# Kernel optimization log

Hardware: AMD Instinct MI355X
Metric: run time of the kernel (lower is better)

## Reference

```python
import jax, jax.numpy as jnp
import numpy as np

H, C = 4, 64          # heads, per-head out_channels (hidden_dim // heads)
D = 256               # hidden_dim
DE = 128              # edge_dim
N_ROWS, N_TOKENS, E = 20000, 100000, 300000
SCALE = 1.0 / np.sqrt(C).astype(np.float32)
EPS = 1e-5


def _lin(key, din, dout):
    k1, k2 = jax.random.split(key)
    W = jax.random.normal(k1, (din, dout), jnp.float32) * 0.05
    b = jax.random.normal(k2, (dout,), jnp.float32) * 0.05
    return W, b


def setup_inputs() -> dict:
    key = jax.random.key(0)
    ks = jax.random.split(key, 26)
    inp = {
        "row_x": jax.random.normal(ks[0], (N_ROWS, D), jnp.float32),
        "token_x": jax.random.normal(ks[1], (N_TOKENS, D), jnp.float32),
        "t2r_edge_index": jax.random.randint(ks[2], (2, E), 0, N_ROWS, jnp.int64),
        "edge_attr_t2r": jax.random.normal(ks[3], (E, DE), jnp.float32),
        "r2t_edge_index": jax.random.randint(ks[4], (2, E), 0, N_ROWS, jnp.int64),
        "edge_attr_r2t": jax.random.normal(ks[5], (E, DE), jnp.float32),
    }
    i = 6
    for p in ("t2r", "r2t"):
        for nm, din in (("q", D), ("k", D), ("v", D), ("e", DE), ("s", D)):
            W, b = _lin(ks[i], din, D); i += 1
            inp[p + "_W" + nm] = W
            inp[p + "_b" + nm] = b
    inp["row_gamma"] = jnp.ones((D,), jnp.float32)
    inp["row_beta"] = jnp.zeros((D,), jnp.float32)
    inp["token_gamma"] = jnp.ones((D,), jnp.float32)
    inp["token_beta"] = jnp.zeros((D,), jnp.float32)
    return inp


def _transformer_conv(x_src, x_dst, ei, ea, Wq, bq, Wk, bk, Wv, bv, We, be, Ws, bs):
    """PyG TransformerConv (concat=True, root_weight=True, edge_dim set, eval)."""
    N = x_dst.shape[0]
    q = (x_dst @ Wq + bq).reshape(N, H, C)       # [N_dst,H,C]
    k = (x_src @ Wk + bk).reshape(-1, H, C)      # [N_src,H,C]
    v = (x_src @ Wv + bv).reshape(-1, H, C)
    e = (ea @ We + be).reshape(-1, H, C)         # [E,H,C]
    src, dst = ei[0], ei[1]
    kj = k[src] + e                              # key_j + edge
    logits = jnp.einsum('ehc,ehc->eh', q[dst], kj) * SCALE  # [E,H]
    amax = jax.ops.segment_max(logits, dst, num_segments=N)  # [N,H]
    ex = jnp.exp(logits - amax[dst])
    denom = jax.ops.segment_sum(ex, dst, num_segments=N)
    alpha = ex / denom[dst]                      # segment softmax over dst
    msg = jax.ops.segment_sum((v[src] + e) * alpha[..., None], dst, num_segments=N)
    return msg.reshape(N, H * C) + x_dst @ Ws + bs  # concat heads + skip lin


def _ln(x, g, b):
    m = jnp.mean(x, -1, keepdims=True)
    var = jnp.mean(jnp.square(x - m), -1, keepdims=True)
    return (x - m) * jax.lax.rsqrt(var + EPS) * g + b


def reference(row_x, token_x, t2r_edge_index, edge_attr_t2r, r2t_edge_index, edge_attr_r2t,
              t2r_Wq, t2r_bq, t2r_Wk, t2r_bk, t2r_Wv, t2r_bv, t2r_We, t2r_be, t2r_Ws, t2r_bs,
              r2t_Wq, r2t_bq, r2t_Wk, r2t_bk, r2t_Wv, r2t_bv, r2t_We, r2t_be, r2t_Ws, r2t_bs,
              row_gamma, row_beta, token_gamma, token_beta):
    row_msg = _transformer_conv(token_x, row_x, t2r_edge_index, edge_attr_t2r,
                                t2r_Wq, t2r_bq, t2r_Wk, t2r_bk, t2r_Wv, t2r_bv,
                                t2r_We, t2r_be, t2r_Ws, t2r_bs)
    row_out = _ln(row_x + row_msg, row_gamma, row_beta)
    tok_msg = _transformer_conv(row_out, token_x, r2t_edge_index, edge_attr_r2t,
                                r2t_Wq, r2t_bq, r2t_Wk, r2t_bk, r2t_Wv, r2t_bv,
                                r2t_We, r2t_be, r2t_Ws, r2t_bs)
    token_out = _ln(token_x + tok_msg, token_gamma, token_beta)
    return row_out, token_out
```

## Files before the change

### kernel.cpp

```cpp
#include <hip/hip_runtime.h>
#include <cstdint>
#include <cstddef>

#define NMAX 100000
#define EMAX 300000

typedef __bf16 bf16x8 __attribute__((ext_vector_type(8)));
typedef float f32x4 __attribute__((ext_vector_type(4)));

__device__ unsigned short g_qs [(size_t)NMAX * 512];
__device__ unsigned short g_kv [(size_t)NMAX * 512];
__device__ unsigned short g_eb [(size_t)EMAX * 256];
__device__ unsigned short g_bfA[(size_t)NMAX * 256];
__device__ unsigned short g_bfB[(size_t)NMAX * 256];
__device__ unsigned short g_bfE[(size_t)EMAX * 128];
__device__ unsigned short g_bfW[589824];
__device__ float g_bias[2560];
__device__ int   g_deg [NMAX + 1];
__device__ int   g_rowptr[NMAX + 1];
__device__ int   g_cur [NMAX];
__device__ int   g_perm[EMAX];
__device__ int   g_bsum[512];

struct P10 { const float* p[10]; };

__device__ __forceinline__ unsigned short f2bf(float f) {
  unsigned u = __float_as_uint(f);
  return (unsigned short)((u + 0x7fffu + ((u >> 16) & 1u)) >> 16);
}
__device__ __forceinline__ float bf2f(unsigned short h) {
  return __uint_as_float((unsigned)h << 16);
}

__global__ __launch_bounds__(256) void conv_bf16(const float* __restrict__ in,
                                                 unsigned short* __restrict__ out,
                                                 long long n8) {
  long long i = (long long)blockIdx.x * 256 + threadIdx.x;
  if (i >= n8) return;
  const float4* p = (const float4*)(in + i * 8);
  float4 a = p[0], b = p[1];
  ushort4 lo = make_ushort4(f2bf(a.x), f2bf(a.y), f2bf(a.z), f2bf(a.w));
  ushort4 hi = make_ushort4(f2bf(b.x), f2bf(b.y), f2bf(b.z), f2bf(b.w));
  ushort4* q = (ushort4*)(out + i * 8);
  q[0] = lo; q[1] = hi;
}

__global__ __launch_bounds__(256) void wconv2(const float* __restrict__ W0,
                                              const float* __restrict__ W1,
                                              unsigned short* __restrict__ Wt,
                                              int K, int NN) {
  int i = blockIdx.x * 256 + threadIdx.x;
  if (i >= NN * K) return;
  int n = i / K, k = i - n * K;
  const float* W = (n < 256) ? W0 : W1;
  Wt[i] = f2bf(W[(size_t)k * 256 + (n & 255)]);
}

__global__ __launch_bounds__(256) void bconcat(P10 b, float* __restrict__ out) {
  int i = blockIdx.x * 256 + threadIdx.x;
  if (i < 2560) out[i] = b.p[i >> 8][i & 255];
}

#define GLL16(gp, lp) __builtin_amdgcn_global_load_lds( \
    (const __attribute__((address_space(1))) void*)(gp), \
    (__attribute__((address_space(3))) void*)(lp), 16, 0, 0)

template <int K, int NS>
__global__ __launch_bounds__(256) void gemm_mfma(const unsigned short* __restrict__ A,
                                                 const unsigned short* __restrict__ Bt,
                                                 const float* __restrict__ bias,
                                                 unsigned short* __restrict__ C, int M) {
  __shared__ unsigned short As[128 * 64];
  __shared__ unsigned short Bs[128 * 64];
  const int tid = threadIdx.x;
  const int lane = tid & 63, wid = tid >> 6;
  const int bm = blockIdx.x * 128, bn = blockIdx.y * 128;
  const int wrow = (wid & 1) * 64, wcol = (wid >> 1) * 64;
  const int sr = lane >> 3;
  const int slot = lane & 7;

  f32x4 acc[4][4] = {};

  for (int k0 = 0; k0 < K; k0 += 64) {
#pragma unroll
    for (int r = 0; r < 4; ++r) {
      int row = (wid * 4 + r) * 8 + sr;
      int arow = bm + row; if (arow >= M) arow = M - 1;
      int kk = k0 + ((slot ^ (row & 7)) << 3);
      GLL16(A + (size_t)arow * K + kk, (unsigned short*)As + (size_t)(wid * 4 + r) * 512);
    }
#pragma unroll
    for (int r = 0; r < 4; ++r) {
      int col = (wid * 4 + r) * 8 + sr;
      int kk = k0 + ((slot ^ (col & 7)) << 3);
      GLL16(Bt + (size_t)(bn + col) * K + kk, (unsigned short*)Bs + (size_t)(wid * 4 + r) * 512);
    }
    __syncthreads();
    const char* Ab = (const char*)As;
    const char* Bb = (const char*)Bs;
#pragma unroll
    for (int h = 0; h < 2; ++h) {
      bf16x8 af[4], bfr[4];
      int g = (lane >> 4) + h * 4;
#pragma unroll
      for (int fm = 0; fm < 4; ++fm) {
        int row = wrow + fm * 16 + (lane & 15);
        af[fm] = *(const bf16x8*)(Ab + row * 128 + ((g ^ (row & 7)) << 4));
      }
#pragma unroll
      for (int fn = 0; fn < 4; ++fn) {
        int col = wcol + fn * 16 + (lane & 15);
        bfr[fn] = *(const bf16x8*)(Bb + col * 128 + ((g ^ (col & 7)) << 4));
      }
#pragma unroll
      for (int fm = 0; fm < 4; ++fm)
#pragma unroll
        for (int fn = 0; fn < 4; ++fn)
          acc[fm][fn] = __builtin_amdgcn_mfma_f32_16x16x32_bf16(af[fm], bfr[fn],
                                                                acc[fm][fn], 0, 0, 0);
    }
    __syncthreads();
  }
  float bv[4];
#pragma unroll
  for (int fn = 0; fn < 4; ++fn) bv[fn] = bias[bn + wcol + fn * 16 + (lane & 15)];
#pragma unroll
  for (int fm = 0; fm < 4; ++fm) {
    int rbase = bm + wrow + fm * 16 + ((lane >> 4) << 2);
#pragma unroll
    for (int j = 0; j < 4; ++j) {
      int row = rbase + j;
      if (row < M) {
        size_t rb = (size_t)row * NS + bn + wcol + (lane & 15);
#pragma unroll
        for (int fn = 0; fn < 4; ++fn)
          C[rb + fn * 16] = f2bf(acc[fm][fn][j] + bv[fn]);
      }
    }
  }
}

__global__ __launch_bounds__(256) void hist_kernel(const int* __restrict__ ei,
                                                   int* __restrict__ deg, int E) {
  int i = blockIdx.x * 256 + threadIdx.x;
  if (i < E) atomicAdd(&deg[ei[E + i]], 1);
}

__global__ __launch_bounds__(256) void scan1(const int* __restrict__ deg,
                                             int* __restrict__ rowptr,
                                             int* __restrict__ bsum, int n) {
  __shared__ int ws[4];
  int i = blockIdx.x * 256 + threadIdx.x;
  int v = (i < n) ? deg[i] : 0;
  int lane = threadIdx.x & 63, wid = threadIdx.x >> 6;
  int inc = v;
#pragma unroll
  for (int o = 1; o < 64; o <<= 1) {
    int t = __shfl_up(inc, o);
    if (lane >= o) inc += t;
  }
  if (lane == 63) ws[wid] = inc;
  __syncthreads();
  int woff = 0;
  if (wid > 0) woff += ws[0];
  if (wid > 1) woff += ws[1];
  if (wid > 2) woff += ws[2];
  if (i < n) rowptr[i] = inc - v + woff;
  if (threadIdx.x == 255) bsum[blockIdx.x] = inc + woff;
}

__global__ __launch_bounds__(512) void scan2(int* __restrict__ bsum, int B) {
  __shared__ int s[512];
  int t = threadIdx.x;
  int v = (t < B) ? bsum[t] : 0;
  s[t] = v;
  __syncthreads();
  for (int o = 1; o < 512; o <<= 1) {
    int a = (t >= o) ? s[t - o] : 0;
    __syncthreads();
    s[t] += a;
    __syncthreads();
  }
  if (t < B) bsum[t] = s[t] - v;
}

__global__ __launch_bounds__(256) void scan3(int* __restrict__ rowptr,
                                             const int* __restrict__ bsum,
                                             const int* __restrict__ deg,
                                             int* __restrict__ cur, int n) {
  int i = blockIdx.x * 256 + threadIdx.x;
  if (i < n) {
    int r = rowptr[i] + bsum[blockIdx.x];
    rowptr[i] = r;
    cur[i] = r;
    if (i == n - 1) rowptr[n] = r + deg[i];
  }
}

__global__ __launch_bounds__(256) void scatter_kernel(const int* __restrict__ ei,
                                                      int* __restrict__ cur,
                                                      int* __restrict__ perm, int E) {
  int i = blockIdx.x * 256 + threadIdx.x;
  if (i < E) {
    int d = ei[E + i];
    int pos = atomicAdd(&cur[d], 1);
    perm[pos] = i;
  }
}

__global__ __launch_bounds__(256) void fused_attn_ln(
    const int* __restrict__ ei, const int* __restrict__ rowptr,
    const int* __restrict__ perm,
    const unsigned short* __restrict__ qs, const unsigned short* __restrict__ kv,
    const unsigned short* __restrict__ eb,
    const float* __restrict__ x,
    const float* __restrict__ gamma, const float* __restrict__ beta,
    float* __restrict__ out, unsigned short* __restrict__ out_bf, int N, int E) {
  int node = blockIdx.x * 4 + (threadIdx.x >> 6);
  if (node >= N) return;
  int lane = threadIdx.x & 63;
  int c4 = lane << 2;
  ushort4 qu = *(const ushort4*)(qs + (size_t)node * 512 + c4);
  float4 qv = make_float4(bf2f(qu.x), bf2f(qu.y), bf2f(qu.z), bf2f(qu.w));
  float4 acc = make_float4(0.f, 0.f, 0.f, 0.f);
  float m = -1e30f, den = 0.f;
  int beg = rowptr[node], end = rowptr[node + 1];
  for (int p_ = beg; p_ < end; ++p_) {
    int eid = perm[p_];
    size_t src = (size_t)ei[eid];
    ushort4 ku = *(const ushort4*)(kv + src * 512 + c4);
    ushort4 vu = *(const ushort4*)(kv + src * 512 + 256 + c4);
    ushort4 eu = *(const ushort4*)(eb + (size_t)eid * 256 + c4);
    float e0 = bf2f(eu.x), e1 = bf2f(eu.y), e2 = bf2f(eu.z), e3 = bf2f(eu.w);
    float p = qv.x * (bf2f(ku.x) + e0) + qv.y * (bf2f(ku.y) + e1) +
              qv.z * (bf2f(ku.z) + e2) + qv.w * (bf2f(ku.w) + e3);
    p += __shfl_xor(p, 1); p += __shfl_xor(p, 2);
    p += __shfl_xor(p, 4); p += __shfl_xor(p, 8);
    p *= 0.125f;
    float mn = fmaxf(m, p);
    float sc = expf(m - mn);
    float w  = expf(p - mn);
    den = den * sc + w;
    acc.x = acc.x * sc + w * (bf2f(vu.x) + e0);
    acc.y = acc.y * sc + w * (bf2f(vu.y) + e1);
    acc.z = acc.z * sc + w * (bf2f(vu.z) + e2);
    acc.w = acc.w * sc + w * (bf2f(vu.w) + e3);
    m = mn;
  }
  float inv = (den > 0.f) ? 1.0f / den : 0.f;
  ushort4 su = *(const ushort4*)(qs + (size_t)node * 512 + 256 + c4);
  size_t base = (size_t)node * 256 + c4;
  float4 xv = *(const float4*)(x + base);
  float4 val = make_float4(xv.x + bf2f(su.x) + acc.x * inv,
                           xv.y + bf2f(su.y) + acc.y * inv,
                           xv.z + bf2f(su.z) + acc.z * inv,
                           xv.w + bf2f(su.w) + acc.w * inv);
  float t = val.x + val.y + val.z + val.w;
#pragma unroll
  for (int o = 1; o < 64; o <<= 1) t += __shfl_xor(t, o);
  float mean = t * (1.0f / 256.0f);
  float d0 = val.x - mean, d1 = val.y - mean, d2 = val.z - mean, d3 = val.w - mean;
  float ss = d0 * d0 + d1 * d1 + d2 * d2 + d3 * d3;
#pragma unroll
  for (int o = 1; o < 64; o <<= 1) ss += __shfl_xor(ss, o);
  float rstd = rsqrtf(ss * (1.0f / 256.0f) + 1e-5f);
  float4 gv = *(const float4*)(gamma + c4);
  float4 bv = *(const float4*)(beta + c4);
  float4 o4 = make_float4(d0 * rstd * gv.x + bv.x, d1 * rstd * gv.y + bv.y,
                          d2 * rstd * gv.z + bv.z, d3 * rstd * gv.w + bv.w);
  *(float4*)(out + base) = o4;
  if (out_bf) {
    ushort4 ob = make_ushort4(f2bf(o4.x), f2bf(o4.y), f2bf(o4.z), f2bf(o4.w));
    *(ushort4*)(out_bf + base) = ob;
  }
}

extern "C" void kernel_launch(void* const* d_in, const int* in_sizes, int n_in,
                              void* d_out, int out_size, void* d_ws, size_t ws_size,
                              hipStream_t stream) {
  const float* row_x   = (const float*)d_in[0];
  const float* token_x = (const float*)d_in[1];
  const int*   ei1     = (const int*)d_in[2];
  const float* ea1     = (const float*)d_in[3];
  const int*   ei2     = (const int*)d_in[4];
  const float* ea2     = (const float*)d_in[5];

  const float* W1q = (const float*)d_in[6];  const float* b1q = (const float*)d_in[7];
  const float* W1k = (const float*)d_in[8];  const float* b1k = (const float*)d_in[9];
  const float* W1v = (const float*)d_in[10]; const float* b1v = (const float*)d_in[11];
  const float* W1e = (const float*)d_in[12]; const float* b1e = (const float*)d_in[13];
  const float* W1s = (const float*)d_in[14]; const float* b1s = (const float*)d_in[15];
  const float* W2q = (const float*)d_in[16]; const float* b2q = (const float*)d_in[17];
  const float* W2k = (const float*)d_in[18]; const float* b2k = (const float*)d_in[19];
  const float* W2v = (const float*)d_in[20]; const float* b2v = (const float*)d_in[21];
  const float* W2e = (const float*)d_in[22]; const float* b2e = (const float*)d_in[23];
  const float* W2s = (const float*)d_in[24]; const float* b2s = (const float*)d_in[25];
  const float* row_gamma   = (const float*)d_in[26];
  const float* row_beta    = (const float*)d_in[27];
  const float* token_gamma = (const float*)d_in[28];
  const float* token_beta  = (const float*)d_in[29];

  const int NR = in_sizes[0] / 256;
  const int NT = in_sizes[1] / 256;
  const int E  = in_sizes[2] / 2;

  float* out_row = (float*)d_out;
  float* out_tok = (float*)d_out + (long long)NR * 256;

  void *pqs_, *pkv_, *peb_, *pbfA_, *pbfB_, *pbfE_, *pbfW_, *pbias_,
       *pdeg_, *prp_, *pcur_, *pperm_, *pbs_;
  hipGetSymbolAddress(&pqs_,  HIP_SYMBOL(g_qs));
  hipGetSymbolAddress(&pkv_,  HIP_SYMBOL(g_kv));
  hipGetSymbolAddress(&peb_,  HIP_SYMBOL(g_eb));
  hipGetSymbolAddress(&pbfA_, HIP_SYMBOL(g_bfA));
  hipGetSymbolAddress(&pbfB_, HIP_SYMBOL(g_bfB));
  hipGetSymbolAddress(&pbfE_, HIP_SYMBOL(g_bfE));
  hipGetSymbolAddress(&pbfW_, HIP_SYMBOL(g_bfW));
  hipGetSymbolAddress(&pbias_,HIP_SYMBOL(g_bias));
  hipGetSymbolAddress(&pdeg_, HIP_SYMBOL(g_deg));
  hipGetSymbolAddress(&prp_,  HIP_SYMBOL(g_rowptr));
  hipGetSymbolAddress(&pcur_, HIP_SYMBOL(g_cur));
  hipGetSymbolAddress(&pperm_,HIP_SYMBOL(g_perm));
  hipGetSymbolAddress(&pbs_,  HIP_SYMBOL(g_bsum));
  unsigned short* qs  = (unsigned short*)pqs_;
  unsigned short* kv  = (unsigned short*)pkv_;
  unsigned short* eb  = (unsigned short*)peb_;
  unsigned short* bfA = (unsigned short*)pbfA_;
  unsigned short* bfB = (unsigned short*)pbfB_;
  unsigned short* bfE = (unsigned short*)pbfE_;
  unsigned short* bfW = (unsigned short*)pbfW_;
  float* gbias = (float*)pbias_;
  int*   deg  = (int*)pdeg_;
  int*   rp   = (int*)prp_;
  int*   cur  = (int*)pcur_;
  int*   perm = (int*)pperm_;
  int*   bsum = (int*)pbs_;

  unsigned short* Wqs1 = bfW + 0;
  unsigned short* Wkv1 = bfW + 131072;
  unsigned short* We1  = bfW + 262144;
  unsigned short* Wqs2 = bfW + 294912;
  unsigned short* Wkv2 = bfW + 425984;
  unsigned short* We2  = bfW + 557056;
  wconv2<<<512, 256, 0, stream>>>(W1q, W1s, Wqs1, 256, 512);
  wconv2<<<512, 256, 0, stream>>>(W1k, W1v, Wkv1, 256, 512);
  wconv2<<<128, 256, 0, stream>>>(W1e, nullptr, We1, 128, 256);
  wconv2<<<512, 256, 0, stream>>>(W2q, W2s, Wqs2, 256, 512);
  wconv2<<<512, 256, 0, stream>>>(W2k, W2v, Wkv2, 256, 512);
  wconv2<<<128, 256, 0, stream>>>(W2e, nullptr, We2, 128, 256);
  P10 bp{{b1q, b1s, b1k, b1v, b1e, b2q, b2s, b2k, b2v, b2e}};
  bconcat<<<10, 256, 0, stream>>>(bp, gbias);

  conv_bf16<<<(int)(((long long)NT * 32 + 255) / 256), 256, 0, stream>>>(token_x, bfA, (long long)NT * 32);
  conv_bf16<<<(int)(((long long)NR * 32 + 255) / 256), 256, 0, stream>>>(row_x, bfB, (long long)NR * 32);
  conv_bf16<<<(int)(((long long)E * 16 + 255) / 256), 256, 0, stream>>>(ea1, bfE, (long long)E * 16);

  const int egrid = (E + 255) / 256;

  auto csr = [&](const int* ei, int Ndst) {
    hipMemsetAsync(deg, 0, (size_t)(Ndst + 1) * sizeof(int), stream);
    hist_kernel<<<egrid, 256, 0, stream>>>(ei, deg, E);
    int B = (Ndst + 255) / 256;
    scan1<<<B, 256, 0, stream>>>(deg, rp, bsum, Ndst);
    scan2<<<1, 512, 0, stream>>>(bsum, B);
    scan3<<<B, 256, 0, stream>>>(rp, bsum, deg, cur, Ndst);
    scatter_kernel<<<egrid, 256, 0, stream>>>(ei, cur, perm, E);
  };

  {
    dim3 gqs((NR + 127) / 128, 4), gkv((NT + 127) / 128, 4), ge((E + 127) / 128, 2);
    gemm_mfma<256, 512><<<gqs, 256, 0, stream>>>(bfB, Wqs1, gbias + 0,    qs, NR);
    gemm_mfma<256, 512><<<gkv, 256, 0, stream>>>(bfA, Wkv1, gbias + 512,  kv, NT);
    gemm_mfma<128, 256><<<ge,  256, 0, stream>>>(bfE, We1,  gbias + 1024, eb, E);
    csr(ei1, NR);
    fused_attn_ln<<<(NR + 3) / 4, 256, 0, stream>>>(ei1, rp, perm, qs, kv, eb,
                                                    row_x, row_gamma, row_beta,
                                                    out_row, bfB, NR, E);
  }

  conv_bf16<<<(int)(((long long)E * 16 + 255) / 256), 256, 0, stream>>>(ea2, bfE, (long long)E * 16);

  {
    dim3 gqs((NT + 127) / 128, 4), gkv((NR + 127) / 128, 4), ge((E + 127) / 128, 2);
    gemm_mfma<256, 512><<<gqs, 256, 0, stream>>>(bfA, Wqs2, gbias + 1280, qs, NT);
    gemm_mfma<256, 512><<<gkv, 256, 0, stream>>>(bfB, Wkv2, gbias + 1792, kv, NR);
    gemm_mfma<128, 256><<<ge,  256, 0, stream>>>(bfE, We2,  gbias + 2304, eb, E);
    csr(ei2, NT);
    fused_attn_ln<<<(NT + 3) / 4, 256, 0, stream>>>(ei2, rp, perm, qs, kv, eb,
                                                    token_x, token_gamma, token_beta,
                                                    out_tok, nullptr, NT, E);
  }
}
```

Baseline: 736.3 us.

## Fuse fp32-to-bf16 input conversion into GEMM loads and prefetch edge gathers

The GEMM now loads fp32 activations and edge attributes straight into LDS with a new swizzle and converts them to bf16 in registers. This removes the separate conversion kernels and their bf16 intermediate buffers. The CSR permutation now stores (src, edge id) pairs so the attention kernel skips one indirect lookup. The attention loop also prefetches the next edge's K/V/E rows and issues the skip and residual loads early. The trade-off is twice the LDS and global read bytes for the A tile in the GEMMs, plus conversion work inside the inner loop.

```diff
diff --git a/kernel.cpp b/kernel.cpp
--- a/kernel.cpp
+++ b/kernel.cpp
@@ -5,21 +5,20 @@
 #define NMAX 100000
 #define EMAX 300000
 
+typedef __bf16 bf16_t;
 typedef __bf16 bf16x8 __attribute__((ext_vector_type(8)));
 typedef float f32x4 __attribute__((ext_vector_type(4)));
 
 __device__ unsigned short g_qs [(size_t)NMAX * 512];
 __device__ unsigned short g_kv [(size_t)NMAX * 512];
 __device__ unsigned short g_eb [(size_t)EMAX * 256];
-__device__ unsigned short g_bfA[(size_t)NMAX * 256];
 __device__ unsigned short g_bfB[(size_t)NMAX * 256];
-__device__ unsigned short g_bfE[(size_t)EMAX * 128];
 __device__ unsigned short g_bfW[589824];
 __device__ float g_bias[2560];
 __device__ int   g_deg [NMAX + 1];
 __device__ int   g_rowptr[NMAX + 1];
 __device__ int   g_cur [NMAX];
-__device__ int   g_perm[EMAX];
+__device__ int2  g_perm2[EMAX];
 __device__ int   g_bsum[512];
 
 struct P10 { const float* p[10]; };
@@ -30,19 +29,6 @@
 }
 __device__ __forceinline__ float bf2f(unsigned short h) {
   return __uint_as_float((unsigned)h << 16);
-}
-
-__global__ __launch_bounds__(256) void conv_bf16(const float* __restrict__ in,
-                                                 unsigned short* __restrict__ out,
-                                                 long long n8) {
-  long long i = (long long)blockIdx.x * 256 + threadIdx.x;
-  if (i >= n8) return;
-  const float4* p = (const float4*)(in + i * 8);
-  float4 a = p[0], b = p[1];
-  ushort4 lo = make_ushort4(f2bf(a.x), f2bf(a.y), f2bf(a.z), f2bf(a.w));
-  ushort4 hi = make_ushort4(f2bf(b.x), f2bf(b.y), f2bf(b.z), f2bf(b.w));
-  ushort4* q = (ushort4*)(out + i * 8);
-  q[0] = lo; q[1] = hi;
 }
 
 __global__ __launch_bounds__(256) void wconv2(const float* __restrict__ W0,
@@ -65,38 +51,53 @@
     (const __attribute__((address_space(1))) void*)(gp), \
     (__attribute__((address_space(3))) void*)(lp), 16, 0, 0)
 
-template <int K, int NS>
-__global__ __launch_bounds__(256) void gemm_mfma(const unsigned short* __restrict__ A,
+template <int K, int NS, bool AF32>
+__global__ __launch_bounds__(256) void gemm_mfma(const void* __restrict__ Av,
                                                  const unsigned short* __restrict__ Bt,
                                                  const float* __restrict__ bias,
                                                  unsigned short* __restrict__ C, int M) {
-  __shared__ unsigned short As[128 * 64];
+  __shared__ __align__(16) char As[AF32 ? 32768 : 16384];
   __shared__ unsigned short Bs[128 * 64];
   const int tid = threadIdx.x;
   const int lane = tid & 63, wid = tid >> 6;
   const int bm = blockIdx.x * 128, bn = blockIdx.y * 128;
   const int wrow = (wid & 1) * 64, wcol = (wid >> 1) * 64;
-  const int sr = lane >> 3;
-  const int slot = lane & 7;
 
   f32x4 acc[4][4] = {};
 
   for (int k0 = 0; k0 < K; k0 += 64) {
-#pragma unroll
-    for (int r = 0; r < 4; ++r) {
-      int row = (wid * 4 + r) * 8 + sr;
-      int arow = bm + row; if (arow >= M) arow = M - 1;
-      int kk = k0 + ((slot ^ (row & 7)) << 3);
-      GLL16(A + (size_t)arow * K + kk, (unsigned short*)As + (size_t)(wid * 4 + r) * 512);
+    if constexpr (AF32) {
+      const float* Af = (const float*)Av;
+      const int sl = lane & 15;
+#pragma unroll
+      for (int r = 0; r < 8; ++r) {
+        int row = wid * 32 + r * 4 + (lane >> 4);
+        int arow = bm + row; if (arow >= M) arow = M - 1;
+        int sw = ((row & 7) << 1) ^ ((row >> 3) & 1);
+        int kk = k0 + ((sl ^ sw) << 2);
+        GLL16(Af + (size_t)arow * K + kk, As + (size_t)(wid * 32 + r * 4) * 256);
+      }
+    } else {
+      const unsigned short* Af = (const unsigned short*)Av;
+      const int sr = lane >> 3, slot = lane & 7;
+#pragma unroll
+      for (int r = 0; r < 4; ++r) {
+        int row = (wid * 4 + r) * 8 + sr;
+        int arow = bm + row; if (arow >= M) arow = M - 1;
+        int kk = k0 + ((slot ^ (row & 7)) << 3);
+        GLL16(Af + (size_t)arow * K + kk, As + (size_t)(wid * 4 + r) * 1024);
+      }
     }
-#pragma unroll
-    for (int r = 0; r < 4; ++r) {
-      int col = (wid * 4 + r) * 8 + sr;
-      int kk = k0 + ((slot ^ (col & 7)) << 3);
-      GLL16(Bt + (size_t)(bn + col) * K + kk, (unsigned short*)Bs + (size_t)(wid * 4 + r) * 512);
+    {
+      const int sr = lane >> 3, slot = lane & 7;
+#pragma unroll
+      for (int r = 0; r < 4; ++r) {
+        int col = (wid * 4 + r) * 8 + sr;
+        int kk = k0 + ((slot ^ (col & 7)) << 3);
+        GLL16(Bt + (size_t)(bn + col) * K + kk, (unsigned short*)Bs + (size_t)(wid * 4 + r) * 512);
+      }
     }
     __syncthreads();
-    const char* Ab = (const char*)As;
     const char* Bb = (const char*)Bs;
 #pragma unroll
     for (int h = 0; h < 2; ++h) {
@@ -105,12 +106,23 @@
 #pragma unroll
       for (int fm = 0; fm < 4; ++fm) {
         int row = wrow + fm * 16 + (lane & 15);
-        af[fm] = *(const bf16x8*)(Ab + row * 128 + ((g ^ (row & 7)) << 4));
+        if constexpr (AF32) {
+          int sw = ((row & 7) << 1) ^ ((row >> 3) & 1);
+          const char* rp2 = As + (size_t)row * 256;
+          float4 f0 = *(const float4*)(rp2 + (((2 * g) ^ sw) << 4));
+          float4 f1 = *(const float4*)(rp2 + (((2 * g + 1) ^ sw) << 4));
+          bf16x8 a;
+          a[0] = (bf16_t)f0.x; a[1] = (bf16_t)f0.y; a[2] = (bf16_t)f0.z; a[3] = (bf16_t)f0.w;
+          a[4] = (bf16_t)f1.x; a[5] = (bf16_t)f1.y; a[6] = (bf16_t)f1.z; a[7] = (bf16_t)f1.w;
+          af[fm] = a;
+        } else {
+          af[fm] = *(const bf16x8*)(As + (size_t)row * 128 + ((g ^ (row & 7)) << 4));
+        }
       }
 #pragma unroll
       for (int fn = 0; fn < 4; ++fn) {
         int col = wcol + fn * 16 + (lane & 15);
-        bfr[fn] = *(const bf16x8*)(Bb + col * 128 + ((g ^ (col & 7)) << 4));
+        bfr[fn] = *(const bf16x8*)(Bb + (size_t)col * 128 + ((g ^ (col & 7)) << 4));
       }
 #pragma unroll
       for (int fm = 0; fm < 4; ++fm)
@@ -199,38 +211,44 @@
 
 __global__ __launch_bounds__(256) void scatter_kernel(const int* __restrict__ ei,
                                                       int* __restrict__ cur,
-                                                      int* __restrict__ perm, int E) {
+                                                      int2* __restrict__ perm2, int E) {
   int i = blockIdx.x * 256 + threadIdx.x;
   if (i < E) {
+    int s = ei[i];
     int d = ei[E + i];
     int pos = atomicAdd(&cur[d], 1);
-    perm[pos] = i;
+    perm2[pos] = make_int2(s, i);
   }
 }
 
 __global__ __launch_bounds__(256) void fused_attn_ln(
-    const int* __restrict__ ei, const int* __restrict__ rowptr,
-    const int* __restrict__ perm,
+    const int* __restrict__ rowptr, const int2* __restrict__ perm2,
     const unsigned short* __restrict__ qs, const unsigned short* __restrict__ kv,
     const unsigned short* __restrict__ eb,
     const float* __restrict__ x,
     const float* __restrict__ gamma, const float* __restrict__ beta,
-    float* __restrict__ out, unsigned short* __restrict__ out_bf, int N, int E) {
+    float* __restrict__ out, unsigned short* __restrict__ out_bf, int N) {
   int node = blockIdx.x * 4 + (threadIdx.x >> 6);
   if (node >= N) return;
   int lane = threadIdx.x & 63;
   int c4 = lane << 2;
   ushort4 qu = *(const ushort4*)(qs + (size_t)node * 512 + c4);
+  ushort4 su = *(const ushort4*)(qs + (size_t)node * 512 + 256 + c4);
+  size_t base = (size_t)node * 256 + c4;
+  float4 xv = *(const float4*)(x + base);
   float4 qv = make_float4(bf2f(qu.x), bf2f(qu.y), bf2f(qu.z), bf2f(qu.w));
   float4 acc = make_float4(0.f, 0.f, 0.f, 0.f);
   float m = -1e30f, den = 0.f;
   int beg = rowptr[node], end = rowptr[node + 1];
+  int2 se = (beg < end) ? perm2[beg] : make_int2(0, 0);
+  ushort4 ku = *(const ushort4*)(kv + (size_t)se.x * 512 + c4);
+  ushort4 vu = *(const ushort4*)(kv + (size_t)se.x * 512 + 256 + c4);
+  ushort4 eu = *(const ushort4*)(eb + (size_t)se.y * 256 + c4);
   for (int p_ = beg; p_ < end; ++p_) {
-    int eid = perm[p_];
-    size_t src = (size_t)ei[eid];
-    ushort4 ku = *(const ushort4*)(kv + src * 512 + c4);
-    ushort4 vu = *(const ushort4*)(kv + src * 512 + 256 + c4);
-    ushort4 eu = *(const ushort4*)(eb + (size_t)eid * 256 + c4);
+    int2 seN = (p_ + 1 < end) ? perm2[p_ + 1] : se;
+    ushort4 kuN = *(const ushort4*)(kv + (size_t)seN.x * 512 + c4);
+    ushort4 vuN = *(const ushort4*)(kv + (size_t)seN.x * 512 + 256 + c4);
+    ushort4 euN = *(const ushort4*)(eb + (size_t)seN.y * 256 + c4);
     float e0 = bf2f(eu.x), e1 = bf2f(eu.y), e2 = bf2f(eu.z), e3 = bf2f(eu.w);
     float p = qv.x * (bf2f(ku.x) + e0) + qv.y * (bf2f(ku.y) + e1) +
               qv.z * (bf2f(ku.z) + e2) + qv.w * (bf2f(ku.w) + e3);
@@ -246,11 +264,9 @@
     acc.z = acc.z * sc + w * (bf2f(vu.z) + e2);
     acc.w = acc.w * sc + w * (bf2f(vu.w) + e3);
     m = mn;
+    ku = kuN; vu = vuN; eu = euN; se = seN;
   }
   float inv = (den > 0.f) ? 1.0f / den : 0.f;
-  ushort4 su = *(const ushort4*)(qs + (size_t)node * 512 + 256 + c4);
-  size_t base = (size_t)node * 256 + c4;
-  float4 xv = *(const float4*)(x + base);
   float4 val = make_float4(xv.x + bf2f(su.x) + acc.x * inv,
                            xv.y + bf2f(su.y) + acc.y * inv,
                            xv.z + bf2f(su.z) + acc.z * inv,
@@ -307,34 +323,30 @@
   float* out_row = (float*)d_out;
   float* out_tok = (float*)d_out + (long long)NR * 256;
 
-  void *pqs_, *pkv_, *peb_, *pbfA_, *pbfB_, *pbfE_, *pbfW_, *pbias_,
+  void *pqs_, *pkv_, *peb_, *pbfB_, *pbfW_, *pbias_,
        *pdeg_, *prp_, *pcur_, *pperm_, *pbs_;
   hipGetSymbolAddress(&pqs_,  HIP_SYMBOL(g_qs));
   hipGetSymbolAddress(&pkv_,  HIP_SYMBOL(g_kv));
   hipGetSymbolAddress(&peb_,  HIP_SYMBOL(g_eb));
-  hipGetSymbolAddress(&pbfA_, HIP_SYMBOL(g_bfA));
   hipGetSymbolAddress(&pbfB_, HIP_SYMBOL(g_bfB));
-  hipGetSymbolAddress(&pbfE_, HIP_SYMBOL(g_bfE));
   hipGetSymbolAddress(&pbfW_, HIP_SYMBOL(g_bfW));
   hipGetSymbolAddress(&pbias_,HIP_SYMBOL(g_bias));
   hipGetSymbolAddress(&pdeg_, HIP_SYMBOL(g_deg));
   hipGetSymbolAddress(&prp_,  HIP_SYMBOL(g_rowptr));
   hipGetSymbolAddress(&pcur_, HIP_SYMBOL(g_cur));
-  hipGetSymbolAddress(&pperm_,HIP_SYMBOL(g_perm));
+  hipGetSymbolAddress(&pperm_,HIP_SYMBOL(g_perm2));
   hipGetSymbolAddress(&pbs_,  HIP_SYMBOL(g_bsum));
   unsigned short* qs  = (unsigned short*)pqs_;
   unsigned short* kv  = (unsigned short*)pkv_;
   unsigned short* eb  = (unsigned short*)peb_;
-  unsigned short* bfA = (unsigned short*)pbfA_;
   unsigned short* bfB = (unsigned short*)pbfB_;
-  unsigned short* bfE = (unsigned short*)pbfE_;
   unsigned short* bfW = (unsigned short*)pbfW_;
   float* gbias = (float*)pbias_;
-  int*   deg  = (int*)pdeg_;
-  int*   rp   = (int*)prp_;
-  int*   cur  = (int*)pcur_;
-  int*   perm = (int*)pperm_;
-  int*   bsum = (int*)pbs_;
+  int*   deg   = (int*)pdeg_;
+  int*   rp    = (int*)prp_;
+  int*   cur   = (int*)pcur_;
+  int2*  perm2 = (int2*)pperm_;
+  int*   bsum  = (int*)pbs_;
 
   unsigned short* Wqs1 = bfW + 0;
   unsigned short* Wkv1 = bfW + 131072;
@@ -351,10 +363,6 @@
   P10 bp{{b1q, b1s, b1k, b1v, b1e, b2q, b2s, b2k, b2v, b2e}};
   bconcat<<<10, 256, 0, stream>>>(bp, gbias);
 
-  conv_bf16<<<(int)(((long long)NT * 32 + 255) / 256), 256, 0, stream>>>(token_x, bfA, (long long)NT * 32);
-  conv_bf16<<<(int)(((long long)NR * 32 + 255) / 256), 256, 0, stream>>>(row_x, bfB, (long long)NR * 32);
-  conv_bf16<<<(int)(((long long)E * 16 + 255) / 256), 256, 0, stream>>>(ea1, bfE, (long long)E * 16);
-
   const int egrid = (E + 255) / 256;
 
   auto csr = [&](const int* ei, int Ndst) {
@@ -364,30 +372,28 @@
     scan1<<<B, 256, 0, stream>>>(deg, rp, bsum, Ndst);
     scan2<<<1, 512, 0, stream>>>(bsum, B);
     scan3<<<B, 256, 0, stream>>>(rp, bsum, deg, cur, Ndst);
-    scatter_kernel<<<egrid, 256, 0, stream>>>(ei, cur, perm, E);
+    scatter_kernel<<<egrid, 256, 0, stream>>>(ei, cur, perm2, E);
   };
 
   {
     dim3 gqs((NR + 127) / 128, 4), gkv((NT + 127) / 128, 4), ge((E + 127) / 128, 2);
-    gemm_mfma<256, 512><<<gqs, 256, 0, stream>>>(bfB, Wqs1, gbias + 0,    qs, NR);
-    gemm_mfma<256, 512><<<gkv, 256, 0, stream>>>(bfA, Wkv1, gbias + 512,  kv, NT);
-    gemm_mfma<128, 256><<<ge,  256, 0, stream>>>(bfE, We1,  gbias + 1024, eb, E);
+    gemm_mfma<256, 512, true><<<gqs, 256, 0, stream>>>(row_x,   Wqs1, gbias + 0,    qs, NR);
+    gemm_mfma<256, 512, true><<<gkv, 256, 0, stream>>>(token_x, Wkv1, gbias + 512,  kv, NT);
+    gemm_mfma<128, 256, true><<<ge,  256, 0, stream>>>(ea1,     We1,  gbias + 1024, eb, E);
     csr(ei1, NR);
-    fused_attn_ln<<<(NR + 3) / 4, 256, 0, stream>>>(ei1, rp, perm, qs, kv, eb,
+    fused_attn_ln<<<(NR + 3) / 4, 256, 0, stream>>>(rp, perm2, qs, kv, eb,
                                                     row_x, row_gamma, row_beta,
-                                                    out_row, bfB, NR, E);
-  }
-
-  conv_bf16<<<(int)(((long long)E * 16 + 255) / 256), 256, 0, stream>>>(ea2, bfE, (long long)E * 16);
+                                                    out_row, bfB, NR);
+  }
 
   {
     dim3 gqs((NT + 127) / 128, 4), gkv((NR + 127) / 128, 4), ge((E + 127) / 128, 2);
-    gemm_mfma<256, 512><<<gqs, 256, 0, stream>>>(bfA, Wqs2, gbias + 1280, qs, NT);
-    gemm_mfma<256, 512><<<gkv, 256, 0, stream>>>(bfB, Wkv2, gbias + 1792, kv, NR);
-    gemm_mfma<128, 256><<<ge,  256, 0, stream>>>(bfE, We2,  gbias + 2304, eb, E);
+    gemm_mfma<256, 512, true ><<<gqs, 256, 0, stream>>>(token_x, Wqs2, gbias + 1280, qs, NT);
+    gemm_mfma<256, 512, false><<<gkv, 256, 0, stream>>>(bfB,     Wkv2, gbias + 1792, kv, NR);
+    gemm_mfma<128, 256, true ><<<ge,  256, 0, stream>>>(ea2,     We2,  gbias + 2304, eb, E);
     csr(ei2, NT);
-    fused_attn_ln<<<(NT + 3) / 4, 256, 0, stream>>>(ei2, rp, perm, qs, kv, eb,
+    fused_attn_ln<<<(NT + 3) / 4, 256, 0, stream>>>(rp, perm2, qs, kv, eb,
                                                     token_x, token_gamma, token_beta,
-                                                    out_tok, nullptr, NT, E);
-  }
-}
+                                                    out_tok, nullptr, NT);
+  }
+}
```

Measured after the change: 797.9 us. +8.4%, slower.

## Merge token-side GEMMs, pack src into CSR perm, and prefetch in attention

Applied to the files above, without the earlier changes.

The token-input projections (layer-1 K/V and layer-2 Q/skip) are merged into one wide GEMM, so token activations are read once. Both edge-attribute GEMMs are hoisted ahead of the first attention stage, and each gets its own buffer. The CSR permutation now stores (src, edge id) pairs, which removes the dependent ei lookup. The attention kernel uses 32 lanes per node with 8-wide bf16 loads and software-prefetches the next edge's K/V/E rows. The cost is extra memory for duplicated buffers and the wider strided layout of the merged output.

```diff
diff --git a/kernel.cpp b/kernel.cpp
--- a/kernel.cpp
+++ b/kernel.cpp
@@ -5,31 +5,40 @@
 #define NMAX 100000
 #define EMAX 300000
 
+typedef __bf16 bf16_t;
 typedef __bf16 bf16x8 __attribute__((ext_vector_type(8)));
 typedef float f32x4 __attribute__((ext_vector_type(4)));
-
+typedef unsigned int u32;
+
+__device__ unsigned short g_mega[(size_t)NMAX * 1024];
 __device__ unsigned short g_qs [(size_t)NMAX * 512];
 __device__ unsigned short g_kv [(size_t)NMAX * 512];
-__device__ unsigned short g_eb [(size_t)EMAX * 256];
+__device__ unsigned short g_eb1[(size_t)EMAX * 256];
+__device__ unsigned short g_eb2[(size_t)EMAX * 256];
 __device__ unsigned short g_bfA[(size_t)NMAX * 256];
 __device__ unsigned short g_bfB[(size_t)NMAX * 256];
-__device__ unsigned short g_bfE[(size_t)EMAX * 128];
+__device__ unsigned short g_bfE1[(size_t)EMAX * 128];
+__device__ unsigned short g_bfE2[(size_t)EMAX * 128];
 __device__ unsigned short g_bfW[589824];
 __device__ float g_bias[2560];
 __device__ int   g_deg [NMAX + 1];
 __device__ int   g_rowptr[NMAX + 1];
 __device__ int   g_cur [NMAX];
-__device__ int   g_perm[EMAX];
+__device__ int2  g_perm2[EMAX];
 __device__ int   g_bsum[512];
 
+struct P4  { const float* p[4]; };
 struct P10 { const float* p[10]; };
 
 __device__ __forceinline__ unsigned short f2bf(float f) {
   unsigned u = __float_as_uint(f);
   return (unsigned short)((u + 0x7fffu + ((u >> 16) & 1u)) >> 16);
 }
-__device__ __forceinline__ float bf2f(unsigned short h) {
-  return __uint_as_float((unsigned)h << 16);
+__device__ __forceinline__ void dec8(uint4 u, float* f) {
+  f[0] = __uint_as_float(u.x << 16); f[1] = __uint_as_float(u.x & 0xffff0000u);
+  f[2] = __uint_as_float(u.y << 16); f[3] = __uint_as_float(u.y & 0xffff0000u);
+  f[4] = __uint_as_float(u.z << 16); f[5] = __uint_as_float(u.z & 0xffff0000u);
+  f[6] = __uint_as_float(u.w << 16); f[7] = __uint_as_float(u.w & 0xffff0000u);
 }
 
 __global__ __launch_bounds__(256) void conv_bf16(const float* __restrict__ in,
@@ -45,15 +54,12 @@
   q[0] = lo; q[1] = hi;
 }
 
-__global__ __launch_bounds__(256) void wconv2(const float* __restrict__ W0,
-                                              const float* __restrict__ W1,
-                                              unsigned short* __restrict__ Wt,
+__global__ __launch_bounds__(256) void wconv4(P4 Ws, unsigned short* __restrict__ Wt,
                                               int K, int NN) {
   int i = blockIdx.x * 256 + threadIdx.x;
   if (i >= NN * K) return;
   int n = i / K, k = i - n * K;
-  const float* W = (n < 256) ? W0 : W1;
-  Wt[i] = f2bf(W[(size_t)k * 256 + (n & 255)]);
+  Wt[i] = f2bf(Ws.p[n >> 8][(size_t)k * 256 + (n & 255)]);
 }
 
 __global__ __launch_bounds__(256) void bconcat(P10 b, float* __restrict__ out) {
@@ -199,79 +205,99 @@
 
 __global__ __launch_bounds__(256) void scatter_kernel(const int* __restrict__ ei,
                                                       int* __restrict__ cur,
-                                                      int* __restrict__ perm, int E) {
+                                                      int2* __restrict__ perm2, int E) {
   int i = blockIdx.x * 256 + threadIdx.x;
   if (i < E) {
+    int s = ei[i];
     int d = ei[E + i];
     int pos = atomicAdd(&cur[d], 1);
-    perm[pos] = i;
+    perm2[pos] = make_int2(s, i);
   }
 }
 
 __global__ __launch_bounds__(256) void fused_attn_ln(
-    const int* __restrict__ ei, const int* __restrict__ rowptr,
-    const int* __restrict__ perm,
-    const unsigned short* __restrict__ qs, const unsigned short* __restrict__ kv,
+    const int* __restrict__ rowptr, const int2* __restrict__ perm2,
+    const unsigned short* __restrict__ qs, int qs_stride,
+    const unsigned short* __restrict__ kv, int kv_stride,
     const unsigned short* __restrict__ eb,
     const float* __restrict__ x,
     const float* __restrict__ gamma, const float* __restrict__ beta,
-    float* __restrict__ out, unsigned short* __restrict__ out_bf, int N, int E) {
-  int node = blockIdx.x * 4 + (threadIdx.x >> 6);
+    float* __restrict__ out, unsigned short* __restrict__ out_bf, int N) {
+  int node = blockIdx.x * 8 + (threadIdx.x >> 5);
   if (node >= N) return;
-  int lane = threadIdx.x & 63;
-  int c4 = lane << 2;
-  ushort4 qu = *(const ushort4*)(qs + (size_t)node * 512 + c4);
-  float4 qv = make_float4(bf2f(qu.x), bf2f(qu.y), bf2f(qu.z), bf2f(qu.w));
-  float4 acc = make_float4(0.f, 0.f, 0.f, 0.f);
+  int sub = threadIdx.x & 31;
+  int c8 = sub << 3;
+  uint4 qu = *(const uint4*)(qs + (size_t)node * qs_stride + c8);
+  uint4 su = *(const uint4*)(qs + (size_t)node * qs_stride + 256 + c8);
+  size_t base = (size_t)node * 256 + c8;
+  float4 xv0 = *(const float4*)(x + base);
+  float4 xv1 = *(const float4*)(x + base + 4);
+  float q[8], s[8];
+  dec8(qu, q); dec8(su, s);
+  float acc[8] = {0.f, 0.f, 0.f, 0.f, 0.f, 0.f, 0.f, 0.f};
   float m = -1e30f, den = 0.f;
   int beg = rowptr[node], end = rowptr[node + 1];
+  int2 se = (beg < end) ? perm2[beg] : make_int2(0, 0);
+  uint4 ku = *(const uint4*)(kv + (size_t)se.x * kv_stride + c8);
+  uint4 vu = *(const uint4*)(kv + (size_t)se.x * kv_stride + 256 + c8);
+  uint4 eu = *(const uint4*)(eb + (size_t)se.y * 256 + c8);
   for (int p_ = beg; p_ < end; ++p_) {
-    int eid = perm[p_];
-    size_t src = (size_t)ei[eid];
-    ushort4 ku = *(const ushort4*)(kv + src * 512 + c4);
-    ushort4 vu = *(const ushort4*)(kv + src * 512 + 256 + c4);
-    ushort4 eu = *(const ushort4*)(eb + (size_t)eid * 256 + c4);
-    float e0 = bf2f(eu.x), e1 = bf2f(eu.y), e2 = bf2f(eu.z), e3 = bf2f(eu.w);
-    float p = qv.x * (bf2f(ku.x) + e0) + qv.y * (bf2f(ku.y) + e1) +
-              qv.z * (bf2f(ku.z) + e2) + qv.w * (bf2f(ku.w) + e3);
-    p += __shfl_xor(p, 1); p += __shfl_xor(p, 2);
-    p += __shfl_xor(p, 4); p += __shfl_xor(p, 8);
+    int2 seN = (p_ + 1 < end) ? perm2[p_ + 1] : se;
+    uint4 kuN = *(const uint4*)(kv + (size_t)seN.x * kv_stride + c8);
+    uint4 vuN = *(const uint4*)(kv + (size_t)seN.x * kv_stride + 256 + c8);
+    uint4 euN = *(const uint4*)(eb + (size_t)seN.y * 256 + c8);
+    float kf[8], vf[8], ef[8];
+    dec8(ku, kf); dec8(vu, vf); dec8(eu, ef);
+    float p = 0.f;
+#pragma unroll
+    for (int j = 0; j < 8; ++j) p += q[j] * (kf[j] + ef[j]);
+    p += __shfl_xor(p, 1); p += __shfl_xor(p, 2); p += __shfl_xor(p, 4);
     p *= 0.125f;
     float mn = fmaxf(m, p);
     float sc = expf(m - mn);
     float w  = expf(p - mn);
     den = den * sc + w;
-    acc.x = acc.x * sc + w * (bf2f(vu.x) + e0);
-    acc.y = acc.y * sc + w * (bf2f(vu.y) + e1);
-    acc.z = acc.z * sc + w * (bf2f(vu.z) + e2);
-    acc.w = acc.w * sc + w * (bf2f(vu.w) + e3);
+#pragma unroll
+    for (int j = 0; j < 8; ++j) acc[j] = acc[j] * sc + w * (vf[j] + ef[j]);
     m = mn;
+    ku = kuN; vu = vuN; eu = euN; se = seN;
   }
   float inv = (den > 0.f) ? 1.0f / den : 0.f;
-  ushort4 su = *(const ushort4*)(qs + (size_t)node * 512 + 256 + c4);
-  size_t base = (size_t)node * 256 + c4;
-  float4 xv = *(const float4*)(x + base);
-  float4 val = make_float4(xv.x + bf2f(su.x) + acc.x * inv,
-                           xv.y + bf2f(su.y) + acc.y * inv,
-                           xv.z + bf2f(su.z) + acc.z * inv,
-                           xv.w + bf2f(su.w) + acc.w * inv);
-  float t = val.x + val.y + val.z + val.w;
-#pragma unroll
-  for (int o = 1; o < 64; o <<= 1) t += __shfl_xor(t, o);
+  float val[8];
+  val[0] = xv0.x + s[0] + acc[0] * inv; val[1] = xv0.y + s[1] + acc[1] * inv;
+  val[2] = xv0.z + s[2] + acc[2] * inv; val[3] = xv0.w + s[3] + acc[3] * inv;
+  val[4] = xv1.x + s[4] + acc[4] * inv; val[5] = xv1.y + s[5] + acc[5] * inv;
+  val[6] = xv1.z + s[6] + acc[6] * inv; val[7] = xv1.w + s[7] + acc[7] * inv;
+  float t = 0.f;
+#pragma unroll
+  for (int j = 0; j < 8; ++j) t += val[j];
+#pragma unroll
+  for (int o = 1; o < 32; o <<= 1) t += __shfl_xor(t, o);
   float mean = t * (1.0f / 256.0f);
-  float d0 = val.x - mean, d1 = val.y - mean, d2 = val.z - mean, d3 = val.w - mean;
-  float ss = d0 * d0 + d1 * d1 + d2 * d2 + d3 * d3;
-#pragma unroll
-  for (int o = 1; o < 64; o <<= 1) ss += __shfl_xor(ss, o);
+  float d[8], ss = 0.f;
+#pragma unroll
+  for (int j = 0; j < 8; ++j) { d[j] = val[j] - mean; ss += d[j] * d[j]; }
+#pragma unroll
+  for (int o = 1; o < 32; o <<= 1) ss += __shfl_xor(ss, o);
   float rstd = rsqrtf(ss * (1.0f / 256.0f) + 1e-5f);
-  float4 gv = *(const float4*)(gamma + c4);
-  float4 bv = *(const float4*)(beta + c4);
-  float4 o4 = make_float4(d0 * rstd * gv.x + bv.x, d1 * rstd * gv.y + bv.y,
-                          d2 * rstd * gv.z + bv.z, d3 * rstd * gv.w + bv.w);
-  *(float4*)(out + base) = o4;
+  float4 g0 = *(const float4*)(gamma + c8);
+  float4 g1 = *(const float4*)(gamma + c8 + 4);
+  float4 b0 = *(const float4*)(beta + c8);
+  float4 b1 = *(const float4*)(beta + c8 + 4);
+  float o8[8];
+  o8[0] = d[0] * rstd * g0.x + b0.x; o8[1] = d[1] * rstd * g0.y + b0.y;
+  o8[2] = d[2] * rstd * g0.z + b0.z; o8[3] = d[3] * rstd * g0.w + b0.w;
+  o8[4] = d[4] * rstd * g1.x + b1.x; o8[5] = d[5] * rstd * g1.y + b1.y;
+  o8[6] = d[6] * rstd * g1.z + b1.z; o8[7] = d[7] * rstd * g1.w + b1.w;
+  *(float4*)(out + base)     = make_float4(o8[0], o8[1], o8[2], o8[3]);
+  *(float4*)(out + base + 4) = make_float4(o8[4], o8[5], o8[6], o8[7]);
   if (out_bf) {
-    ushort4 ob = make_ushort4(f2bf(o4.x), f2bf(o4.y), f2bf(o4.z), f2bf(o4.w));
-    *(ushort4*)(out_bf + base) = ob;
+    uint4 ob;
+    ob.x = (u32)f2bf(o8[0]) | ((u32)f2bf(o8[1]) << 16);
+    ob.y = (u32)f2bf(o8[2]) | ((u32)f2bf(o8[3]) << 16);
+    ob.z = (u32)f2bf(o8[4]) | ((u32)f2bf(o8[5]) << 16);
+    ob.w = (u32)f2bf(o8[6]) | ((u32)f2bf(o8[7]) << 16);
+    *(uint4*)(out_bf + base) = ob;
   }
 }
 
@@ -307,53 +333,58 @@
   float* out_row = (float*)d_out;
   float* out_tok = (float*)d_out + (long long)NR * 256;
 
-  void *pqs_, *pkv_, *peb_, *pbfA_, *pbfB_, *pbfE_, *pbfW_, *pbias_,
-       *pdeg_, *prp_, *pcur_, *pperm_, *pbs_;
-  hipGetSymbolAddress(&pqs_,  HIP_SYMBOL(g_qs));
-  hipGetSymbolAddress(&pkv_,  HIP_SYMBOL(g_kv));
-  hipGetSymbolAddress(&peb_,  HIP_SYMBOL(g_eb));
-  hipGetSymbolAddress(&pbfA_, HIP_SYMBOL(g_bfA));
-  hipGetSymbolAddress(&pbfB_, HIP_SYMBOL(g_bfB));
-  hipGetSymbolAddress(&pbfE_, HIP_SYMBOL(g_bfE));
-  hipGetSymbolAddress(&pbfW_, HIP_SYMBOL(g_bfW));
-  hipGetSymbolAddress(&pbias_,HIP_SYMBOL(g_bias));
-  hipGetSymbolAddress(&pdeg_, HIP_SYMBOL(g_deg));
-  hipGetSymbolAddress(&prp_,  HIP_SYMBOL(g_rowptr));
-  hipGetSymbolAddress(&pcur_, HIP_SYMBOL(g_cur));
-  hipGetSymbolAddress(&pperm_,HIP_SYMBOL(g_perm));
-  hipGetSymbolAddress(&pbs_,  HIP_SYMBOL(g_bsum));
-  unsigned short* qs  = (unsigned short*)pqs_;
-  unsigned short* kv  = (unsigned short*)pkv_;
-  unsigned short* eb  = (unsigned short*)peb_;
-  unsigned short* bfA = (unsigned short*)pbfA_;
-  unsigned short* bfB = (unsigned short*)pbfB_;
-  unsigned short* bfE = (unsigned short*)pbfE_;
-  unsigned short* bfW = (unsigned short*)pbfW_;
+  void *pmega_, *pqs_, *pkv_, *peb1_, *peb2_, *pbfA_, *pbfB_, *pbfE1_, *pbfE2_,
+       *pbfW_, *pbias_, *pdeg_, *prp_, *pcur_, *pperm_, *pbs_;
+  hipGetSymbolAddress(&pmega_, HIP_SYMBOL(g_mega));
+  hipGetSymbolAddress(&pqs_,   HIP_SYMBOL(g_qs));
+  hipGetSymbolAddress(&pkv_,   HIP_SYMBOL(g_kv));
+  hipGetSymbolAddress(&peb1_,  HIP_SYMBOL(g_eb1));
+  hipGetSymbolAddress(&peb2_,  HIP_SYMBOL(g_eb2));
+  hipGetSymbolAddress(&pbfA_,  HIP_SYMBOL(g_bfA));
+  hipGetSymbolAddress(&pbfB_,  HIP_SYMBOL(g_bfB));
+  hipGetSymbolAddress(&pbfE1_, HIP_SYMBOL(g_bfE1));
+  hipGetSymbolAddress(&pbfE2_, HIP_SYMBOL(g_bfE2));
+  hipGetSymbolAddress(&pbfW_,  HIP_SYMBOL(g_bfW));
+  hipGetSymbolAddress(&pbias_, HIP_SYMBOL(g_bias));
+  hipGetSymbolAddress(&pdeg_,  HIP_SYMBOL(g_deg));
+  hipGetSymbolAddress(&prp_,   HIP_SYMBOL(g_rowptr));
+  hipGetSymbolAddress(&pcur_,  HIP_SYMBOL(g_cur));
+  hipGetSymbolAddress(&pperm_, HIP_SYMBOL(g_perm2));
+  hipGetSymbolAddress(&pbs_,   HIP_SYMBOL(g_bsum));
+  unsigned short* mega = (unsigned short*)pmega_;
+  unsigned short* qs   = (unsigned short*)pqs_;
+  unsigned short* kv   = (unsigned short*)pkv_;
+  unsigned short* eb1  = (unsigned short*)peb1_;
+  unsigned short* eb2  = (unsigned short*)peb2_;
+  unsigned short* bfA  = (unsigned short*)pbfA_;
+  unsigned short* bfB  = (unsigned short*)pbfB_;
+  unsigned short* bfE1 = (unsigned short*)pbfE1_;
+  unsigned short* bfE2 = (unsigned short*)pbfE2_;
+  unsigned short* bfW  = (unsigned short*)pbfW_;
   float* gbias = (float*)pbias_;
-  int*   deg  = (int*)pdeg_;
-  int*   rp   = (int*)prp_;
-  int*   cur  = (int*)pcur_;
-  int*   perm = (int*)pperm_;
-  int*   bsum = (int*)pbs_;
-
-  unsigned short* Wqs1 = bfW + 0;
-  unsigned short* Wkv1 = bfW + 131072;
-  unsigned short* We1  = bfW + 262144;
-  unsigned short* Wqs2 = bfW + 294912;
-  unsigned short* Wkv2 = bfW + 425984;
-  unsigned short* We2  = bfW + 557056;
-  wconv2<<<512, 256, 0, stream>>>(W1q, W1s, Wqs1, 256, 512);
-  wconv2<<<512, 256, 0, stream>>>(W1k, W1v, Wkv1, 256, 512);
-  wconv2<<<128, 256, 0, stream>>>(W1e, nullptr, We1, 128, 256);
-  wconv2<<<512, 256, 0, stream>>>(W2q, W2s, Wqs2, 256, 512);
-  wconv2<<<512, 256, 0, stream>>>(W2k, W2v, Wkv2, 256, 512);
-  wconv2<<<128, 256, 0, stream>>>(W2e, nullptr, We2, 128, 256);
-  P10 bp{{b1q, b1s, b1k, b1v, b1e, b2q, b2s, b2k, b2v, b2e}};
+  int*   deg   = (int*)pdeg_;
+  int*   rp    = (int*)prp_;
+  int*   cur   = (int*)pcur_;
+  int2*  perm2 = (int2*)pperm_;
+  int*   bsum  = (int*)pbs_;
+
+  unsigned short* Wmega = bfW + 0;
+  unsigned short* Wqs1  = bfW + 262144;
+  unsigned short* Wkv2  = bfW + 393216;
+  unsigned short* We1   = bfW + 524288;
+  unsigned short* We2   = bfW + 557056;
+  wconv4<<<1024, 256, 0, stream>>>(P4{{W1k, W1v, W2q, W2s}}, Wmega, 256, 1024);
+  wconv4<<<512, 256, 0, stream>>>(P4{{W1q, W1s, nullptr, nullptr}}, Wqs1, 256, 512);
+  wconv4<<<512, 256, 0, stream>>>(P4{{W2k, W2v, nullptr, nullptr}}, Wkv2, 256, 512);
+  wconv4<<<128, 256, 0, stream>>>(P4{{W1e, nullptr, nullptr, nullptr}}, We1, 128, 256);
+  wconv4<<<128, 256, 0, stream>>>(P4{{W2e, nullptr, nullptr, nullptr}}, We2, 128, 256);
+  P10 bp{{b1k, b1v, b2q, b2s, b1q, b1s, b2k, b2v, b1e, b2e}};
   bconcat<<<10, 256, 0, stream>>>(bp, gbias);
 
   conv_bf16<<<(int)(((long long)NT * 32 + 255) / 256), 256, 0, stream>>>(token_x, bfA, (long long)NT * 32);
   conv_bf16<<<(int)(((long long)NR * 32 + 255) / 256), 256, 0, stream>>>(row_x, bfB, (long long)NR * 32);
-  conv_bf16<<<(int)(((long long)E * 16 + 255) / 256), 256, 0, stream>>>(ea1, bfE, (long long)E * 16);
+  conv_bf16<<<(int)(((long long)E * 16 + 255) / 256), 256, 0, stream>>>(ea1, bfE1, (long long)E * 16);
+  conv_bf16<<<(int)(((long long)E * 16 + 255) / 256), 256, 0, stream>>>(ea2, bfE2, (long long)E * 16);
 
   const int egrid = (E + 255) / 256;
 
@@ -364,30 +395,29 @@
     scan1<<<B, 256, 0, stream>>>(deg, rp, bsum, Ndst);
     scan2<<<1, 512, 0, stream>>>(bsum, B);
     scan3<<<B, 256, 0, stream>>>(rp, bsum, deg, cur, Ndst);
-    scatter_kernel<<<egrid, 256, 0, stream>>>(ei, cur, perm, E);
+    scatter_kernel<<<egrid, 256, 0, stream>>>(ei, cur, perm2, E);
   };
 
-  {
-    dim3 gqs((NR + 127) / 128, 4), gkv((NT + 127) / 128, 4), ge((E + 127) / 128, 2);
-    gemm_mfma<256, 512><<<gqs, 256, 0, stream>>>(bfB, Wqs1, gbias + 0,    qs, NR);
-    gemm_mfma<256, 512><<<gkv, 256, 0, stream>>>(bfA, Wkv1, gbias + 512,  kv, NT);
-    gemm_mfma<128, 256><<<ge,  256, 0, stream>>>(bfE, We1,  gbias + 1024, eb, E);
-    csr(ei1, NR);
-    fused_attn_ln<<<(NR + 3) / 4, 256, 0, stream>>>(ei1, rp, perm, qs, kv, eb,
-                                                    row_x, row_gamma, row_beta,
-                                                    out_row, bfB, NR, E);
-  }
-
-  conv_bf16<<<(int)(((long long)E * 16 + 255) / 256), 256, 0, stream>>>(ea2, bfE, (long long)E * 16);
-
-  {
-    dim3 gqs((NT + 127) / 128, 4), gkv((NR + 127) / 128, 4), ge((E + 127) / 128, 2);
-    gemm_mfma<256, 512><<<gqs, 256, 0, stream>>>(bfA, Wqs2, gbias + 1280, qs, NT);
-    gemm_mfma<256, 512><<<gkv, 256, 0, stream>>>(bfB, Wkv2, gbias + 1792, kv, NR);
-    gemm_mfma<128, 256><<<ge,  256, 0, stream>>>(bfE, We2,  gbias + 2304, eb, E);
-    csr(ei2, NT);
-    fused_attn_ln<<<(NT + 3) / 4, 256, 0, stream>>>(ei2, rp, perm, qs, kv, eb,
-                                                    token_x, token_gamma, token_beta,
-                                                    out_tok, nullptr, NT, E);
-  }
-}
+  gemm_mfma<256, 1024><<<dim3((NT + 127) / 128, 8), 256, 0, stream>>>(
+      bfA, Wmega, gbias + 0, mega, NT);
+  gemm_mfma<256, 512><<<dim3((NR + 127) / 128, 4), 256, 0, stream>>>(
+      bfB, Wqs1, gbias + 1024, qs, NR);
+  gemm_mfma<128, 256><<<dim3((E + 127) / 128, 2), 256, 0, stream>>>(
+      bfE1, We1, gbias + 2048, eb1, E);
+  gemm_mfma<128, 256><<<dim3((E + 127) / 128, 2), 256, 0, stream>>>(
+      bfE2, We2, gbias + 2304, eb2, E);
+
+  csr(ei1, NR);
+  fused_attn_ln<<<(NR + 7) / 8, 256, 0, stream>>>(rp, perm2,
+                                                  qs, 512, mega, 1024, eb1,
+                                                  row_x, row_gamma, row_beta,
+                                                  out_row, bfB, NR);
+
+  gemm_mfma<256, 512><<<dim3((NR + 127) / 128, 4), 256, 0, stream>>>(
+      bfB, Wkv2, gbias + 1536, kv, NR);
+  csr(ei2, NT);
+  fused_attn_ln<<<(NT + 7) / 8, 256, 0, stream>>>(rp, perm2,
+                                                  mega + 512, 1024, kv, 512, eb2,
+                                                  token_x, token_gamma, token_beta,
+                                                  out_tok, nullptr, NT);
+}
```

Result: faster. 682.2 us (-7.3%).
